# Kernel optimization log

Hardware: AMD Instinct MI355X
Metric: run time of the kernel (lower is better)

Reference implementation:

```python
import jax, jax.numpy as jnp
import numpy as np

LAMBDA_A = 1.0
NUM_ITER = 3
K = 64
BN_EPS = 1e-5


def setup_inputs() -> dict:
    key = jax.random.key(0)
    ks = jax.random.split(key, 8)
    B, C, H, W = 16, 512, 64, 64
    x = jax.random.normal(ks[0], (B, C, H, W), dtype=jnp.float32)
    # codebook mu: init normal(std~sqrt(2/k)) then L2-normalize along dim=1 (k axis), as in torch init
    mu = jax.random.normal(ks[1], (C, K), dtype=jnp.float32) * np.sqrt(2.0 / K)
    mu = mu / jnp.maximum(jnp.linalg.norm(mu, axis=1, keepdims=True), 1e-12)
    # 1x1 convs expressed as (out, in) matrices
    stem_w = jax.random.normal(ks[2], (C, C), dtype=jnp.float32) * np.sqrt(2.0 / C)
    stem_b = jnp.zeros((C,), dtype=jnp.float32)
    head_w = jax.random.normal(ks[3], (C, C), dtype=jnp.float32) * np.sqrt(2.0 / C)
    head_b = jnp.zeros((C,), dtype=jnp.float32)
    bn_gamma = jnp.ones((C,), dtype=jnp.float32)
    bn_beta = jnp.zeros((C,), dtype=jnp.float32)
    return {"x": x, "mu": mu, "stem_w": stem_w, "stem_b": stem_b,
            "head_w": head_w, "head_b": head_b,
            "bn_gamma": bn_gamma, "bn_beta": bn_beta}


def _conv1x1(x, w, b):
    # x: (B,C,H,W), w: (O,C)
    return jnp.einsum('bchw,oc->bohw', x, w) + b[None, :, None, None]


def reference(x, mu, stem_w, stem_b, head_w, head_b, bn_gamma, bn_beta):
    B, C, H, W = x.shape
    N = H * W
    y = _conv1x1(x, stem_w, stem_b)                 # (B,C,H,W)
    yf = y.reshape(B, C, N).transpose(0, 2, 1)      # (B,N,C)

    mu_b = jnp.broadcast_to(mu[None], (B, C, K))    # (B,C,K)
    z = None
    for _ in range(NUM_ITER):
        z = jax.nn.softmax(LAMBDA_A * jnp.einsum('bnc,bck->bnk', yf, mu_b), axis=2)
        zn = z / (1e-6 + z.sum(axis=1, keepdims=True))
        mu_b = jnp.einsum('bnc,bnk->bck', yf, zn)
        mu_b = mu_b / jnp.maximum(jnp.linalg.norm(mu_b, axis=1, keepdims=True), 1e-12)

    # EM loop runs under no_grad in torch
    mu_b = jax.lax.stop_gradient(mu_b)
    z = jax.lax.stop_gradient(z)

    y2 = jnp.einsum('bck,bnk->bcn', mu_b, z).reshape(B, C, H, W)

    # head: ReLU -> 1x1 conv -> BatchNorm2d (training-mode batch stats)
    h = _conv1x1(jnp.maximum(y2, 0.0), head_w, head_b)
    mean = h.mean(axis=(0, 2, 3), keepdims=True)
    var = h.var(axis=(0, 2, 3), keepdims=True)
    h = (h - mean) * jax.lax.rsqrt(var + BN_EPS)
    h = h * bn_gamma[None, :, None, None] + bn_beta[None, :, None, None]

    return jnp.maximum(h + x, 0.0)
```

## Files before the change

### kernel.cpp

```cpp
#include <hip/hip_runtime.h>


typedef _Float16 half_t;
typedef _Float16 half4 __attribute__((ext_vector_type(4)));
typedef _Float16 half8 __attribute__((ext_vector_type(8)));
typedef float f32x4 __attribute__((ext_vector_type(4)));

#define GLD_LDS(gp, lp) __builtin_amdgcn_global_load_lds( \
    (const __attribute__((address_space(1))) void*)(gp),  \
    (__attribute__((address_space(3))) void*)(lp), 16, 0, 0)

constexpr int CB = 16;
constexpr int CC = 512;
constexpr int CN = 4096;
constexpr int CKK = 64;
constexpr long MALL = (long)CB * CN;

__device__ inline int swz8(int bid, int n) {
  return (bid & 7) * (n >> 3) + (bid >> 3);
}

__global__ __launch_bounds__(256) void prep(
    const float* __restrict__ stem_w, const float* __restrict__ head_w,
    const float* __restrict__ mu,
    half_t* __restrict__ swh, half_t* __restrict__ hwh,
    half_t* __restrict__ muT, half_t* __restrict__ muck)
{
  int i = blockIdx.x * 256 + threadIdx.x;
  swh[i] = (half_t)stem_w[i];
  hwh[i] = (half_t)head_w[i];
  if (i < CC * CKK) {
    int c = i >> 6, k = i & 63;
    half_t v = (half_t)mu[i];
    for (int b = 0; b < CB; ++b) {
      muT[(long)b * CKK * CC + (long)k * CC + c] = v;
      muck[(long)b * CC * CKK + i] = v;
    }
  }
}

__global__ __launch_bounds__(256) void xpose(
    const float* __restrict__ in, half_t* __restrict__ outT)
{
  __shared__ half_t t[64][65];
  const int s0 = blockIdx.x * 64, r0 = blockIdx.y * 64;
  const long bz = blockIdx.z;
  const float* ib = in + bz * (long)CC * CN;
  half_t* ob = outT + bz * (long)CC * CN;
  const int tid = threadIdx.x, cl = tid & 63, rw = tid >> 6;
#pragma unroll
  for (int it = 0; it < 16; ++it) {
    int r = it * 4 + rw;
    t[cl][r] = (half_t)ib[(long)(r0 + r) * CN + s0 + cl];
  }
  __syncthreads();
#pragma unroll
  for (int it = 0; it < 16; ++it) {
    int s = it * 4 + rw;
    ob[(long)(s0 + s) * CC + r0 + cl] = t[s][cl];
  }
}

template <int BM, int BN, int MODE, int EPI, bool SWZ>
__global__ __launch_bounds__(256) void gemm_abt(
    const half_t* __restrict__ A, const half_t* __restrict__ Bm,
    half_t* __restrict__ Co, half_t* __restrict__ CoT,
    float* __restrict__ Cacc, const float* __restrict__ bias,
    int M, int Nn, int Kk, int ksplit, long sA, long sB, long sC)
{
  constexpr int FM = BM / 32, FN = BN / 32;
  constexpr int HB = (BM + BN) * 64;
  constexpr int STG = 2 * HB;
  constexpr int EPS = (EPI != 0) ? BN * (BM + 4) : 0;
  constexpr int TOT = STG > EPS ? STG : EPS;
  __shared__ __align__(16) half_t smem[TOT];

  const int tid = threadIdx.x, wid = tid >> 6, lane = tid & 63;
  int bid = blockIdx.x;
  if constexpr (SWZ) bid = swz8(bid, gridDim.x);
  const int tilesN = Nn / BN;
  const int tm = bid / tilesN, tn = bid % tilesN;
  const long bz = blockIdx.z;
  const half_t* Ab = A + bz * sA + (long)tm * BM * Kk;
  const half_t* Bb = Bm + bz * sB + (long)tn * BN * Kk;
  const int ksteps = Kk >> 6;
  const int per = ksteps / ksplit;
  const int ks0 = blockIdx.y * per, ks1 = ks0 + per;
  const int wr = wid >> 1, wc = wid & 1;

  auto stage = [&](int ks, int buf) {
    half_t* dA = smem + buf * HB;
    half_t* dB = dA + BM * 64;
    const half_t* ga = Ab + (long)ks * 64;
#pragma unroll
    for (int c = wid; c < BM / 8; c += 4)
      GLD_LDS(ga + (long)(c * 8 + (lane >> 3)) * Kk + (lane & 7) * 8, &dA[c * 512]);
    const half_t* gb = Bb + (long)ks * 64;
#pragma unroll
    for (int c = wid; c < BN / 8; c += 4)
      GLD_LDS(gb + (long)(c * 8 + (lane >> 3)) * Kk + (lane & 7) * 8, &dB[c * 512]);
  };

  f32x4 acc[FM][FN];
#pragma unroll
  for (int i = 0; i < FM; ++i)
#pragma unroll
    for (int j = 0; j < FN; ++j) acc[i][j] = f32x4{0.f, 0.f, 0.f, 0.f};

  stage(ks0, 0);
  __syncthreads();
  int cur = 0;
  for (int ks = ks0; ks < ks1; ++ks) {
    if (ks + 1 < ks1) stage(ks + 1, cur ^ 1);
    const half_t* lA = smem + cur * HB;
    const half_t* lB = lA + BM * 64;
#pragma unroll
    for (int kk = 0; kk < 2; ++kk) {
      half8 af[FM], bfr[FN];
#pragma unroll
      for (int i = 0; i < FM; ++i)
        af[i] = *(const half8*)&lA[(wr * (BM / 2) + i * 16 + (lane & 15)) * 64 +
                                   kk * 32 + (lane >> 4) * 8];
#pragma unroll
      for (int j = 0; j < FN; ++j)
        bfr[j] = *(const half8*)&lB[(wc * (BN / 2) + j * 16 + (lane & 15)) * 64 +
                                    kk * 32 + (lane >> 4) * 8];
#pragma unroll
      for (int i = 0; i < FM; ++i)
#pragma unroll
        for (int j = 0; j < FN; ++j)
          acc[i][j] = __builtin_amdgcn_mfma_f32_16x16x32_f16(af[i], bfr[j],
                                                             acc[i][j], 0, 0, 0);
    }
    __syncthreads();
    cur ^= 1;
  }

  if constexpr (EPI != 0) {
    static_assert(BM == 128 && BN == 128, "LDS epilogue assumes 128x128");
    constexpr int PIT = BM + 4;
    half_t* ep = smem;
#pragma unroll
    for (int j = 0; j < FN; ++j) {
      const int nl = wc * 64 + j * 16 + (lane & 15);
      float bv = 0.f;
      if constexpr (MODE & 1) bv = bias[tn * BN + nl];
#pragma unroll
      for (int i = 0; i < FM; ++i) {
        const int ml = wr * 64 + i * 16 + ((lane >> 4) << 2);
        half4 h;
#pragma unroll
        for (int r = 0; r < 4; ++r) {
          float v = acc[i][j][r] + bv;
          if constexpr (MODE & 2) v = fmaxf(v, 0.f);
          h[r] = (half_t)v;
        }
        *(half4*)&ep[nl * PIT + ml] = h;
      }
    }
    __syncthreads();
    const long rowbase = (long)tm * BM;
    if constexpr (EPI & 1) {
#pragma unroll
      for (int s = 0; s < 8; ++s) {
        const int q = tid + 256 * s;
        const int m = q & 127, cc = q >> 7;
        half8 v;
#pragma unroll
        for (int e = 0; e < 8; ++e) v[e] = ep[(cc * 8 + e) * PIT + m];
        *(half8*)&Co[bz * sC + (rowbase + m) * Nn + tn * BN + cc * 8] = v;
      }
    }
    if constexpr (EPI & 2) {
      const long b = rowbase >> 12, nbase = rowbase & 4095;
#pragma unroll
      for (int s = 0; s < 8; ++s) {
        const int q = tid + 256 * s;
        const int mc = q & 15;
        const int cl = q >> 4;
        half8 v = *(const half8*)&ep[cl * PIT + mc * 8];
        *(half8*)&CoT[(b * Nn + tn * BN + cl) * 4096 + nbase + mc * 8] = v;
      }
    }
  } else {
#pragma unroll
    for (int j = 0; j < FN; ++j) {
      const int n = tn * BN + wc * (BN / 2) + j * 16 + (lane & 15);
      float bv = 0.f;
      if constexpr (MODE & 1) bv = bias[n];
#pragma unroll
      for (int i = 0; i < FM; ++i) {
        const int mbase = tm * BM + wr * (BM / 2) + i * 16 + ((lane >> 4) << 2);
#pragma unroll
        for (int r = 0; r < 4; ++r) {
          const long idx = bz * sC + (long)(mbase + r) * Nn + n;
          if constexpr ((MODE & 4) != 0) {
            atomicAdd(&Cacc[idx], acc[i][j][r]);
          } else {
            float v = acc[i][j][r] + bv;
            if constexpr ((MODE & 2) != 0) v = fmaxf(v, 0.f);
            Co[idx] = (half_t)v;
          }
        }
      }
    }
  }
}

__global__ __launch_bounds__(256) void s_softmax(
    const half_t* __restrict__ Yf, const half_t* __restrict__ muT,
    half_t* __restrict__ zp, half_t* __restrict__ zT)
{
  constexpr int HB = (128 + 64) * 64;
  __shared__ __align__(16) union {
    half_t st[2 * HB];
    half_t zh[128 * 68];
  } sm;
  const int tid = threadIdx.x, wid = tid >> 6, lane = tid & 63;
  const int tm = blockIdx.x;
  const long bz = blockIdx.z;
  const half_t* Ab = Yf + bz * (long)CN * CC + (long)tm * 128 * CC;
  const half_t* Bb = muT + bz * (long)CKK * CC;

  auto stage = [&](int ks, int buf) {
    half_t* dA = sm.st + buf * HB;
    half_t* dB = dA + 128 * 64;
    const half_t* ga = Ab + (long)ks * 64;
#pragma unroll
    for (int c = wid; c < 16; c += 4)
      GLD_LDS(ga + (long)(c * 8 + (lane >> 3)) * CC + (lane & 7) * 8, &dA[c * 512]);
    const half_t* gb = Bb + (long)ks * 64;
#pragma unroll
    for (int c = wid; c < 8; c += 4)
      GLD_LDS(gb + (long)(c * 8 + (lane >> 3)) * CC + (lane & 7) * 8, &dB[c * 512]);
  };

  f32x4 acc[2][4];
#pragma unroll
  for (int i = 0; i < 2; ++i)
#pragma unroll
    for (int j = 0; j < 4; ++j) acc[i][j] = f32x4{0.f, 0.f, 0.f, 0.f};

  stage(0, 0);
  __syncthreads();
  int cur = 0;
  for (int ks = 0; ks < 8; ++ks) {
    if (ks + 1 < 8) stage(ks + 1, cur ^ 1);
    const half_t* lA = sm.st + cur * HB;
    const half_t* lB = lA + 128 * 64;
#pragma unroll
    for (int kk = 0; kk < 2; ++kk) {
      half8 af[2], bfr[4];
#pragma unroll
      for (int i = 0; i < 2; ++i)
        af[i] = *(const half8*)&lA[(wid * 32 + i * 16 + (lane & 15)) * 64 +
                                   kk * 32 + (lane >> 4) * 8];
#pragma unroll
      for (int j = 0; j < 4; ++j)
        bfr[j] = *(const half8*)&lB[(j * 16 + (lane & 15)) * 64 +
                                    kk * 32 + (lane >> 4) * 8];
#pragma unroll
      for (int i = 0; i < 2; ++i)
#pragma unroll
        for (int j = 0; j < 4; ++j)
          acc[i][j] = __builtin_amdgcn_mfma_f32_16x16x32_f16(af[i], bfr[j],
                                                             acc[i][j], 0, 0, 0);
    }
    __syncthreads();
    cur ^= 1;
  }

#pragma unroll
  for (int i = 0; i < 2; ++i)
#pragma unroll
    for (int r = 0; r < 4; ++r) {
      float mx = fmaxf(fmaxf(acc[i][0][r], acc[i][1][r]),
                       fmaxf(acc[i][2][r], acc[i][3][r]));
#pragma unroll
      for (int m = 1; m < 16; m <<= 1) mx = fmaxf(mx, __shfl_xor(mx, m));
      float p[4], s = 0.f;
#pragma unroll
      for (int j = 0; j < 4; ++j) { p[j] = __expf(acc[i][j][r] - mx); s += p[j]; }
#pragma unroll
      for (int m = 1; m < 16; m <<= 1) s += __shfl_xor(s, m);
      const float inv = 1.f / s;
#pragma unroll
      for (int j = 0; j < 4; ++j) acc[i][j][r] = p[j] * inv;
    }

#pragma unroll
  for (int i = 0; i < 2; ++i)
#pragma unroll
    for (int j = 0; j < 4; ++j)
#pragma unroll
      for (int r = 0; r < 4; ++r) {
        const int row = wid * 32 + i * 16 + ((lane >> 4) << 2) + r;
        const int col = j * 16 + (lane & 15);
        sm.zh[row * 68 + col] = (half_t)acc[i][j][r];
      }
  __syncthreads();
  if (zp) {
    const int nl = tid >> 1, seg = tid & 1;
    const long base = bz * (long)CN * CKK + (long)(tm * 128 + nl) * CKK + seg * 32;
#pragma unroll
    for (int g = 0; g < 4; ++g) {
      half8 v;
#pragma unroll
      for (int e = 0; e < 8; ++e) v[e] = sm.zh[nl * 68 + seg * 32 + g * 8 + e];
      *(half8*)&zp[base + g * 8] = v;
    }
  }
  {
    const int k = tid >> 2, seg = tid & 3;
    const long base = bz * (long)CKK * CN + (long)k * CN + tm * 128 + seg * 32;
#pragma unroll
    for (int g = 0; g < 4; ++g) {
      half8 v;
#pragma unroll
      for (int e = 0; e < 8; ++e) v[e] = sm.zh[(seg * 32 + g * 8 + e) * 68 + k];
      *(half8*)&zT[base + g * 8] = v;
    }
  }
}

__global__ __launch_bounds__(64) void mu_norm(
    const float* __restrict__ acc, half_t* __restrict__ muT, half_t* __restrict__ muck)
{
  const int bk = blockIdx.x;
  const int b = bk >> 6, k = bk & 63;
  const float* row = acc + (long)bk * CC;
  const int t = threadIdx.x;
  float v[8]; float s = 0.f;
#pragma unroll
  for (int e = 0; e < 8; ++e) { v[e] = row[t * 8 + e]; s += v[e] * v[e]; }
#pragma unroll
  for (int m = 1; m < 64; m <<= 1) s += __shfl_xor(s, m);
  const float inv = 1.f / fmaxf(sqrtf(s), 1e-12f);
  half8 o;
#pragma unroll
  for (int e = 0; e < 8; ++e) o[e] = (half_t)(v[e] * inv);
  *(half8*)&muT[(long)bk * CC + t * 8] = o;
  half_t* mc = muck + (long)b * CC * CKK;
#pragma unroll
  for (int e = 0; e < 8; ++e) mc[(long)(t * 8 + e) * CKK + k] = o[e];
}

__global__ __launch_bounds__(256) void bn_stats2(
    const half_t* __restrict__ hcn, float* __restrict__ stats)
{
  const int c = blockIdx.x, tid = threadIdx.x;
  float s = 0.f, s2 = 0.f;
  for (int b = 0; b < CB; ++b) {
    const half_t* p = hcn + ((long)b * CC + c) * CN;
    for (int i = tid * 8; i < CN; i += 2048) {
      half8 v = *(const half8*)&p[i];
#pragma unroll
      for (int e = 0; e < 8; ++e) { float f = (float)v[e]; s += f; s2 += f * f; }
    }
  }
#pragma unroll
  for (int m = 1; m < 64; m <<= 1) { s += __shfl_xor(s, m); s2 += __shfl_xor(s2, m); }
  __shared__ float r[8];
  const int wid = tid >> 6;
  if ((tid & 63) == 0) { r[wid] = s; r[4 + wid] = s2; }
  __syncthreads();
  if (tid == 0) {
    stats[c] = r[0] + r[1] + r[2] + r[3];
    stats[CC + c] = r[4] + r[5] + r[6] + r[7];
  }
}

__global__ void bn_param(const float* __restrict__ stats,
                         const float* __restrict__ gamma, const float* __restrict__ beta,
                         float* __restrict__ scsh)
{
  const int c = threadIdx.x;
  const float cnt = 1.f / 65536.f;
  const float mean = stats[c] * cnt;
  const float var = stats[CC + c] * cnt - mean * mean;
  const float sc = gamma[c] * rsqrtf(var + 1e-5f);
  scsh[c] = sc;
  scsh[CC + c] = beta[c] - mean * sc;
}

__global__ __launch_bounds__(256) void bn_final2(
    const half_t* __restrict__ hcn, const float* __restrict__ x,
    const float* __restrict__ scsh, float* __restrict__ out)
{
  const long i8 = (long)blockIdx.x * 256 + threadIdx.x;
  const int c = (int)((i8 >> 9) & 511);
  const float sc = scsh[c], sh = scsh[CC + c];
  half8 h = *(const half8*)&hcn[i8 * 8];
  f32x4 x0 = *(const f32x4*)&x[i8 * 8];
  f32x4 x1 = *(const f32x4*)&x[i8 * 8 + 4];
  f32x4 o0, o1;
#pragma unroll
  for (int e = 0; e < 4; ++e) o0[e] = fmaxf((float)h[e] * sc + sh + x0[e], 0.f);
#pragma unroll
  for (int e = 0; e < 4; ++e) o1[e] = fmaxf((float)h[4 + e] * sc + sh + x1[e], 0.f);
  *(f32x4*)&out[i8 * 8] = o0;
  *(f32x4*)&out[i8 * 8 + 4] = o1;
}

extern "C" void kernel_launch(void* const* d_in, const int* in_sizes, int n_in,
                              void* d_out, int out_size, void* d_ws, size_t ws_size,
                              hipStream_t stream)
{
  const float* x      = (const float*)d_in[0];
  const float* mu     = (const float*)d_in[1];
  const float* stem_w = (const float*)d_in[2];
  const float* stem_b = (const float*)d_in[3];
  const float* head_w = (const float*)d_in[4];
  const float* head_b = (const float*)d_in[5];
  const float* bn_g   = (const float*)d_in[6];
  const float* bn_b   = (const float*)d_in[7];
  float* out = (float*)d_out;

  const size_t NEED = 214ull << 20;
  if (ws_size < NEED) {
    hipMemsetAsync(d_out, 0, (size_t)out_size * 4, stream);
    return;
  }
  char* ws = (char*)d_ws;
  const long MB = 1 << 20;
  half_t* xT   = (half_t*)(ws);
  half_t* Yf   = (half_t*)(ws + 64 * MB);
  half_t* ycn  = (half_t*)(ws + 128 * MB);
  half_t* z    = (half_t*)(ws + 192 * MB);
  half_t* zT   = (half_t*)(ws + 200 * MB);
  half_t* muT  = (half_t*)(ws + 208 * MB);
  half_t* muck = (half_t*)(ws + 209 * MB);
  float* muacc = (float*)(ws + 210 * MB);
  half_t* swh  = (half_t*)(ws + 212 * MB);
  half_t* hwh  = (half_t*)(ws + 212 * MB + 512 * 1024);
  float* stats = (float*)(ws + 213 * MB);
  float* scsh  = (float*)(ws + 213 * MB + 8 * 1024);
  half_t* y2f = xT;
  half_t* hcn = Yf;

  prep<<<1024, 256, 0, stream>>>(stem_w, head_w, mu, swh, hwh, muT, muck);
  xpose<<<dim3(64, 8, 16), 256, 0, stream>>>(x, xT);
  gemm_abt<128, 128, 1, 3, true><<<dim3(2048, 1, 1), 256, 0, stream>>>(
      xT, swh, Yf, ycn, nullptr, stem_b, (int)MALL, CC, CC, 1, 0, 0, 0);

  for (int it = 0; it < 3; ++it) {
    s_softmax<<<dim3(32, 1, 16), 256, 0, stream>>>(
        Yf, muT, (it == 2) ? z : nullptr, zT);
    hipMemsetAsync(muacc, 0, (size_t)CB * CKK * CC * 4, stream);
    gemm_abt<64, 128, 4, 0, false><<<dim3(4, 4, 16), 256, 0, stream>>>(
        zT, ycn, nullptr, nullptr, muacc, nullptr, CKK, CC, CN, 4,
        (long)CKK * CN, (long)CC * CN, (long)CKK * CC);
    mu_norm<<<CB * CKK, 64, 0, stream>>>(muacc, muT, muck);
  }
  gemm_abt<128, 128, 2, 1, true><<<dim3(128, 1, 16), 256, 0, stream>>>(
      z, muck, y2f, nullptr, nullptr, nullptr, CN, CC, CKK, 1,
      (long)CN * CKK, (long)CC * CKK, (long)CN * CC);
  gemm_abt<128, 128, 1, 2, true><<<dim3(2048, 1, 1), 256, 0, stream>>>(
      y2f, hwh, nullptr, hcn, nullptr, head_b, (int)MALL, CC, CC, 1, 0, 0, 0);

  bn_stats2<<<CC, 256, 0, stream>>>(hcn, stats);
  bn_param<<<1, 512, 0, stream>>>(stats, bn_g, bn_b, scsh);
  bn_final2<<<16384, 256, 0, stream>>>(hcn, x, scsh, out);
}
```

Before: 431.0 us.

## XOR-swizzle LDS tiles and deepen GEMM pipeline with explicit vmcnt waits

Applies an XOR swizzle on 16-byte column groups when loading tiles via global_load_lds and reading them back, to avoid LDS bank conflicts in the MFMA fragment loads. Restructures the K loop in the generic GEMM and the softmax GEMM to keep two stages in flight, using explicit s_waitcnt vmcnt counts and raw barriers instead of __syncthreads. Raises wave priority around the MFMA blocks. The hardcoded vmcnt values must match the number of loads per stage, or reads could race.

```diff
diff --git a/kernel.cpp b/kernel.cpp
--- a/kernel.cpp
+++ b/kernel.cpp
@@ -9,6 +9,15 @@
 #define GLD_LDS(gp, lp) __builtin_amdgcn_global_load_lds( \
     (const __attribute__((address_space(1))) void*)(gp),  \
     (__attribute__((address_space(3))) void*)(lp), 16, 0, 0)
+
+#define SBAR __builtin_amdgcn_sched_barrier(0)
+#define RAWBAR do { SBAR; __builtin_amdgcn_s_barrier(); SBAR; } while (0)
+
+template <int L> __device__ __forceinline__ void vmwait() {
+  if constexpr (L == 8) asm volatile("s_waitcnt vmcnt(8)" ::: "memory");
+  else if constexpr (L == 6) asm volatile("s_waitcnt vmcnt(6)" ::: "memory");
+  else asm volatile("s_waitcnt vmcnt(0)" ::: "memory");
+}
 
 constexpr int CB = 16;
 constexpr int CC = 512;
@@ -70,6 +79,7 @@
 {
   constexpr int FM = BM / 32, FN = BN / 32;
   constexpr int HB = (BM + BN) * 64;
+  constexpr int LCNT = (BM / 8) / 4 + (BN / 8) / 4;
   constexpr int STG = 2 * HB;
   constexpr int EPS = (EPI != 0) ? BN * (BM + 4) : 0;
   constexpr int TOT = STG > EPS ? STG : EPS;
@@ -88,17 +98,20 @@
   const int ks0 = blockIdx.y * per, ks1 = ks0 + per;
   const int wr = wid >> 1, wc = wid & 1;
 
+  const int r8 = lane >> 3;
+  const int gcs = ((lane & 7) ^ r8) * 8;
+
   auto stage = [&](int ks, int buf) {
     half_t* dA = smem + buf * HB;
     half_t* dB = dA + BM * 64;
     const half_t* ga = Ab + (long)ks * 64;
 #pragma unroll
     for (int c = wid; c < BM / 8; c += 4)
-      GLD_LDS(ga + (long)(c * 8 + (lane >> 3)) * Kk + (lane & 7) * 8, &dA[c * 512]);
+      GLD_LDS(ga + (long)(c * 8 + r8) * Kk + gcs, &dA[c * 512]);
     const half_t* gb = Bb + (long)ks * 64;
 #pragma unroll
     for (int c = wid; c < BN / 8; c += 4)
-      GLD_LDS(gb + (long)(c * 8 + (lane >> 3)) * Kk + (lane & 7) * 8, &dB[c * 512]);
+      GLD_LDS(gb + (long)(c * 8 + r8) * Kk + gcs, &dB[c * 512]);
   };
 
   f32x4 acc[FM][FN];
@@ -108,31 +121,42 @@
     for (int j = 0; j < FN; ++j) acc[i][j] = f32x4{0.f, 0.f, 0.f, 0.f};
 
   stage(ks0, 0);
-  __syncthreads();
+  if (ks0 + 1 < ks1) { stage(ks0 + 1, 1); vmwait<LCNT>(); }
+  else               { vmwait<0>(); }
+  RAWBAR;
+
   int cur = 0;
   for (int ks = ks0; ks < ks1; ++ks) {
-    if (ks + 1 < ks1) stage(ks + 1, cur ^ 1);
     const half_t* lA = smem + cur * HB;
     const half_t* lB = lA + BM * 64;
 #pragma unroll
     for (int kk = 0; kk < 2; ++kk) {
       half8 af[FM], bfr[FN];
-#pragma unroll
-      for (int i = 0; i < FM; ++i)
-        af[i] = *(const half8*)&lA[(wr * (BM / 2) + i * 16 + (lane & 15)) * 64 +
-                                   kk * 32 + (lane >> 4) * 8];
-#pragma unroll
-      for (int j = 0; j < FN; ++j)
-        bfr[j] = *(const half8*)&lB[(wc * (BN / 2) + j * 16 + (lane & 15)) * 64 +
-                                    kk * 32 + (lane >> 4) * 8];
+      const int cg = kk * 4 + (lane >> 4);
+#pragma unroll
+      for (int i = 0; i < FM; ++i) {
+        const int rA = wr * (BM / 2) + i * 16 + (lane & 15);
+        af[i] = *(const half8*)&lA[rA * 64 + ((cg ^ (rA & 7)) << 3)];
+      }
+#pragma unroll
+      for (int j = 0; j < FN; ++j) {
+        const int rB = wc * (BN / 2) + j * 16 + (lane & 15);
+        bfr[j] = *(const half8*)&lB[rB * 64 + ((cg ^ (rB & 7)) << 3)];
+      }
+      __builtin_amdgcn_s_setprio(1);
 #pragma unroll
       for (int i = 0; i < FM; ++i)
 #pragma unroll
         for (int j = 0; j < FN; ++j)
           acc[i][j] = __builtin_amdgcn_mfma_f32_16x16x32_f16(af[i], bfr[j],
                                                              acc[i][j], 0, 0, 0);
-    }
-    __syncthreads();
+      __builtin_amdgcn_s_setprio(0);
+    }
+    RAWBAR;
+    const bool more = (ks + 2 < ks1);
+    if (more) { stage(ks + 2, cur); vmwait<LCNT>(); }
+    else      { vmwait<0>(); }
+    RAWBAR;
     cur ^= 1;
   }
 
@@ -222,17 +246,20 @@
   const half_t* Ab = Yf + bz * (long)CN * CC + (long)tm * 128 * CC;
   const half_t* Bb = muT + bz * (long)CKK * CC;
 
+  const int r8 = lane >> 3;
+  const int gcs = ((lane & 7) ^ r8) * 8;
+
   auto stage = [&](int ks, int buf) {
     half_t* dA = sm.st + buf * HB;
     half_t* dB = dA + 128 * 64;
     const half_t* ga = Ab + (long)ks * 64;
 #pragma unroll
     for (int c = wid; c < 16; c += 4)
-      GLD_LDS(ga + (long)(c * 8 + (lane >> 3)) * CC + (lane & 7) * 8, &dA[c * 512]);
+      GLD_LDS(ga + (long)(c * 8 + r8) * CC + gcs, &dA[c * 512]);
     const half_t* gb = Bb + (long)ks * 64;
 #pragma unroll
     for (int c = wid; c < 8; c += 4)
-      GLD_LDS(gb + (long)(c * 8 + (lane >> 3)) * CC + (lane & 7) * 8, &dB[c * 512]);
+      GLD_LDS(gb + (long)(c * 8 + r8) * CC + gcs, &dB[c * 512]);
   };
 
   f32x4 acc[2][4];
@@ -242,31 +269,41 @@
     for (int j = 0; j < 4; ++j) acc[i][j] = f32x4{0.f, 0.f, 0.f, 0.f};
 
   stage(0, 0);
-  __syncthreads();
+  stage(1, 1);
+  vmwait<6>();
+  RAWBAR;
   int cur = 0;
   for (int ks = 0; ks < 8; ++ks) {
-    if (ks + 1 < 8) stage(ks + 1, cur ^ 1);
     const half_t* lA = sm.st + cur * HB;
     const half_t* lB = lA + 128 * 64;
 #pragma unroll
     for (int kk = 0; kk < 2; ++kk) {
       half8 af[2], bfr[4];
-#pragma unroll
-      for (int i = 0; i < 2; ++i)
-        af[i] = *(const half8*)&lA[(wid * 32 + i * 16 + (lane & 15)) * 64 +
-                                   kk * 32 + (lane >> 4) * 8];
-#pragma unroll
-      for (int j = 0; j < 4; ++j)
-        bfr[j] = *(const half8*)&lB[(j * 16 + (lane & 15)) * 64 +
-                                    kk * 32 + (lane >> 4) * 8];
+      const int cg = kk * 4 + (lane >> 4);
+#pragma unroll
+      for (int i = 0; i < 2; ++i) {
+        const int rA = wid * 32 + i * 16 + (lane & 15);
+        af[i] = *(const half8*)&lA[rA * 64 + ((cg ^ (rA & 7)) << 3)];
+      }
+#pragma unroll
+      for (int j = 0; j < 4; ++j) {
+        const int rB = j * 16 + (lane & 15);
+        bfr[j] = *(const half8*)&lB[rB * 64 + ((cg ^ (rB & 7)) << 3)];
+      }
+      __builtin_amdgcn_s_setprio(1);
 #pragma unroll
       for (int i = 0; i < 2; ++i)
 #pragma unroll
         for (int j = 0; j < 4; ++j)
           acc[i][j] = __builtin_amdgcn_mfma_f32_16x16x32_f16(af[i], bfr[j],
                                                              acc[i][j], 0, 0, 0);
-    }
-    __syncthreads();
+      __builtin_amdgcn_s_setprio(0);
+    }
+    RAWBAR;
+    const bool more = (ks + 2 < 8);
+    if (more) { stage(ks + 2, cur); vmwait<6>(); }
+    else      { vmwait<0>(); }
+    RAWBAR;
     cur ^= 1;
   }
 
```

New measurement: 411.6 us. 1.05x faster.
